# Optimization experiments

Measured on AMD Instinct MI355X. Metric: run time of the kernel, lower is better.

Reference implementation:

```python
import jax, jax.numpy as jnp
import numpy as np

B, S, D = 64, 2048, 512


def setup_inputs() -> dict:
    key = jax.random.key(0)
    ks = jax.random.split(key, 6)
    scale = 1.0 / np.sqrt(D)
    return {
        "source": jax.random.normal(ks[0], (B, D), jnp.float32),
        "memory_bank": jax.random.normal(ks[1], (B, S, D), jnp.float32),
        "memory_lengths": jax.random.randint(ks[2], (B,), 1, S + 1, jnp.int64),
        "Wq": jax.random.normal(ks[3], (D, D), jnp.float32) * scale,
        "bq": jnp.zeros((D,), jnp.float32),
        "Wc": jax.random.normal(ks[4], (D, D), jnp.float32) * scale,
        "v": jax.random.normal(ks[5], (D,), jnp.float32) * scale,
    }


def reference(source, memory_bank, memory_lengths, Wq, bq, Wc, v):
    # Bahdanau (mlp) score: v^T tanh(Wq q + Uc h_j); one_step (tgt_len=1).
    wq = source @ Wq.T + bq                     # [B, D]
    uh = jnp.einsum("bsd,ed->bse", memory_bank, Wc)  # [B, S, D]
    scores = jnp.einsum("bsd,d->bs", jnp.tanh(wq[:, None, :] + uh), v)  # [B, S]
    mask = jnp.arange(S)[None, :] < memory_lengths[:, None]  # [B, S]
    scores = jnp.where(mask, scores, -jnp.inf)
    align = jax.nn.softmax(scores, axis=-1)      # [B, S]
    c = jnp.einsum("bs,bsd->bd", align, memory_bank)  # [B, D] (no_concat=True, mlp -> no tanh)
    return c, align
```

## Files before the change

kernel.cpp:

```cpp
#include <hip/hip_runtime.h>

#define NB 64
#define NS 2048
#define ND 512

typedef short s16x8 __attribute__((ext_vector_type(8)));
typedef float f32x16 __attribute__((ext_vector_type(16)));

__device__ __forceinline__ unsigned short bf16_rnd(float x){
  union { float f; unsigned u; } c; c.f = x;
  unsigned r = c.u + 0x7FFFu + ((c.u >> 16) & 1u);
  return (unsigned short)(r >> 16);
}
__device__ __forceinline__ float bf16f(unsigned short h){
  union { unsigned u; float f; } c; c.u = ((unsigned)h) << 16;
  return c.f;
}
__device__ __forceinline__ float fast_tanh(float x){
  float e = __expf(2.0f * x);
  return 1.0f - 2.0f / (e + 1.0f);
}

__global__ void k_prep_wc(const float* __restrict__ Wc, unsigned short* __restrict__ wcf){
  int t  = blockIdx.x * 256 + threadIdx.x;
  int l  = t & 63;
  int n  = (t >> 6) & 15;
  int ks = t >> 10;
  int e  = n * 32 + (l & 31);
  int d0 = ks * 16 + ((l >> 5) * 8);
  const float4* g4 = (const float4*)(Wc + (size_t)e * ND + d0);
  float4 x0 = g4[0], x1 = g4[1];
  float xs[8] = {x0.x,x0.y,x0.z,x0.w,x1.x,x1.y,x1.z,x1.w};
  s16x8 hv, lv;
#pragma unroll
  for(int j=0;j<8;j++){
    float x = xs[j];
    unsigned short h = bf16_rnd(x);
    hv[j] = (short)h;
    lv[j] = (short)bf16_rnd(x - bf16f(h));
  }
  size_t base = ((size_t)(ks*16 + n))*1024 + (size_t)l*8;
  *(s16x8*)(wcf + base)       = hv;
  *(s16x8*)(wcf + base + 512) = lv;
}

__global__ void k_wq(const float* __restrict__ src, const float* __restrict__ Wq,
                     const float* __restrict__ bq, float* __restrict__ wq){
  __shared__ float s_src[ND];
  int b = blockIdx.x;
  for(int i=threadIdx.x;i<ND;i+=256) s_src[i] = src[(size_t)b*ND + i];
  __syncthreads();
  for(int e=threadIdx.x; e<ND; e+=256){
    const float4* wr = (const float4*)(Wq + (size_t)e*ND);
    float acc = 0.f;
#pragma unroll 4
    for(int i=0;i<ND/4;i++){
      float4 w4 = wr[i];
      acc += w4.x*s_src[4*i] + w4.y*s_src[4*i+1] + w4.z*s_src[4*i+2] + w4.w*s_src[4*i+3];
    }
    wq[(size_t)b*ND + e] = acc + bq[e];
  }
}

__launch_bounds__(512, 2)
__global__ void k_scores(const float* __restrict__ mb, const unsigned short* __restrict__ wcf,
                         const float* __restrict__ wq, const float* __restrict__ v,
                         float* __restrict__ scores){
  __shared__ unsigned short a_lds[2*32*2*64*8];
  __shared__ float wq_s[ND];
  __shared__ float v_s[ND];
  __shared__ float sred[8][64];

  int b  = blockIdx.x >> 5;
  int sc = blockIdx.x & 31;
  int s0 = sc * 64;
  int tid = threadIdx.x;
  int w = tid >> 6;
  int l = tid & 63;

  if(tid < ND){ wq_s[tid] = wq[(size_t)b*ND + tid]; v_s[tid] = v[tid]; }

  const float* mbb = mb + ((size_t)b*NS + s0) * ND;
#pragma unroll
  for(int i=0;i<8;i++){
    int flat = w + 8*i;
    int mt = flat >> 5;
    int ks = flat & 31;
    int r  = mt*32 + (l & 31);
    int k0 = ks*16 + ((l >> 5) * 8);
    const float4* g4 = (const float4*)(mbb + (size_t)r*ND + k0);
    float4 x0 = g4[0], x1 = g4[1];
    float xs[8] = {x0.x,x0.y,x0.z,x0.w,x1.x,x1.y,x1.z,x1.w};
    s16x8 hv, lv;
#pragma unroll
    for(int j=0;j<8;j++){
      float x = xs[j];
      unsigned short h = bf16_rnd(x);
      hv[j] = (short)h;
      lv[j] = (short)bf16_rnd(x - bf16f(h));
    }
    int base = (((mt*32 + ks)*2)*64 + l) * 8;
    *(s16x8*)(a_lds + base)       = hv;
    *(s16x8*)(a_lds + base + 512) = lv;
  }
  __syncthreads();

  const s16x8* aptr = (const s16x8*)a_lds;
  const s16x8* bptr = (const s16x8*)wcf;

  f32x16 acc[2][2];
#pragma unroll
  for(int mt=0;mt<2;mt++)
#pragma unroll
    for(int nt=0;nt<2;nt++)
#pragma unroll
      for(int q=0;q<16;q++) acc[mt][nt][q] = 0.f;

  int n0 = w * 2;
#pragma unroll 2
  for(int ks=0;ks<32;ks++){
    s16x8 a0h = aptr[       ks*128      + l];
    s16x8 a0l = aptr[       ks*128 + 64 + l];
    s16x8 a1h = aptr[4096 + ks*128      + l];
    s16x8 a1l = aptr[4096 + ks*128 + 64 + l];
    const s16x8* bp = bptr + ((size_t)ks*16 + n0)*128 + l;
    s16x8 b0h = bp[0];
    s16x8 b0l = bp[64];
    s16x8 b1h = bp[128];
    s16x8 b1l = bp[192];

    acc[0][0] = __builtin_amdgcn_mfma_f32_32x32x16_bf16(a0h, b0h, acc[0][0], 0,0,0);
    acc[1][0] = __builtin_amdgcn_mfma_f32_32x32x16_bf16(a1h, b0h, acc[1][0], 0,0,0);
    acc[0][1] = __builtin_amdgcn_mfma_f32_32x32x16_bf16(a0h, b1h, acc[0][1], 0,0,0);
    acc[1][1] = __builtin_amdgcn_mfma_f32_32x32x16_bf16(a1h, b1h, acc[1][1], 0,0,0);
    acc[0][0] = __builtin_amdgcn_mfma_f32_32x32x16_bf16(a0h, b0l, acc[0][0], 0,0,0);
    acc[1][0] = __builtin_amdgcn_mfma_f32_32x32x16_bf16(a1h, b0l, acc[1][0], 0,0,0);
    acc[0][1] = __builtin_amdgcn_mfma_f32_32x32x16_bf16(a0h, b1l, acc[0][1], 0,0,0);
    acc[1][1] = __builtin_amdgcn_mfma_f32_32x32x16_bf16(a1h, b1l, acc[1][1], 0,0,0);
    acc[0][0] = __builtin_amdgcn_mfma_f32_32x32x16_bf16(a0l, b0h, acc[0][0], 0,0,0);
    acc[1][0] = __builtin_amdgcn_mfma_f32_32x32x16_bf16(a1l, b0h, acc[1][0], 0,0,0);
    acc[0][1] = __builtin_amdgcn_mfma_f32_32x32x16_bf16(a0l, b1h, acc[0][1], 0,0,0);
    acc[1][1] = __builtin_amdgcn_mfma_f32_32x32x16_bf16(a1l, b1h, acc[1][1], 0,0,0);
  }

  float sp[2][16];
#pragma unroll
  for(int mt=0;mt<2;mt++)
#pragma unroll
    for(int r=0;r<16;r++) sp[mt][r] = 0.f;

#pragma unroll
  for(int nt=0;nt<2;nt++){
    int e = (n0 + nt)*32 + (l & 31);
    float wqe = wq_s[e];
    float ve  = v_s[e];
#pragma unroll
    for(int mt=0;mt<2;mt++)
#pragma unroll
      for(int r=0;r<16;r++){
        float th = fast_tanh(acc[mt][nt][r] + wqe);
        sp[mt][r] += ve * th;
      }
  }

#pragma unroll
  for(int o=1;o<32;o<<=1){
#pragma unroll
    for(int mt=0;mt<2;mt++)
#pragma unroll
      for(int r=0;r<16;r++)
        sp[mt][r] += __shfl_xor(sp[mt][r], o, 64);
  }

  if((l & 31) == 0){
    int half = l >> 5;
#pragma unroll
    for(int mt=0;mt<2;mt++)
#pragma unroll
      for(int r=0;r<16;r++){
        int row = mt*32 + (r&3) + 8*(r>>2) + 4*half;
        sred[w][row] = sp[mt][r];
      }
  }
  __syncthreads();
  if(tid < 64){
    float s = 0.f;
#pragma unroll
    for(int ww=0;ww<8;ww++) s += sred[ww][tid];
    scores[(size_t)b*NS + s0 + tid] = s;
  }
}

__global__ void k_softmax(const float* __restrict__ scores, const unsigned* __restrict__ lraw,
                          float* __restrict__ align){
  __shared__ float red[4];
  int b = blockIdx.x, tid = threadIdx.x;
  bool is64 = (lraw[1] == 0u);
  int len = (int)(is64 ? lraw[2*b] : lraw[b]);

  float loc[8];
  float mx = -1e30f;
#pragma unroll
  for(int i=0;i<8;i++){
    int s = tid + i*256;
    float val = scores[(size_t)b*NS + s];
    loc[i] = (s < len) ? val : -1e30f;
    mx = fmaxf(mx, loc[i]);
  }
#pragma unroll
  for(int o=1;o<64;o<<=1) mx = fmaxf(mx, __shfl_xor(mx, o, 64));
  if((tid & 63) == 0) red[tid >> 6] = mx;
  __syncthreads();
  mx = fmaxf(fmaxf(red[0],red[1]), fmaxf(red[2],red[3]));
  __syncthreads();

  float sum = 0.f;
#pragma unroll
  for(int i=0;i<8;i++){
    int s = tid + i*256;
    loc[i] = (s < len) ? __expf(loc[i] - mx) : 0.f;
    sum += loc[i];
  }
#pragma unroll
  for(int o=1;o<64;o<<=1) sum += __shfl_xor(sum, o, 64);
  if((tid & 63) == 0) red[tid >> 6] = sum;
  __syncthreads();
  sum = red[0] + red[1] + red[2] + red[3];
  float inv = 1.f / sum;
#pragma unroll
  for(int i=0;i<8;i++){
    int s = tid + i*256;
    align[(size_t)b*NS + s] = loc[i] * inv;
  }
}

__global__ void k_context(const float* __restrict__ mb, const float* __restrict__ align,
                          float* __restrict__ c){
  int b  = blockIdx.x >> 4;
  int sc = blockIdx.x & 15;
  int s0 = sc * 128;
  int d0 = threadIdx.x * 2;
  const float* base = mb + ((size_t)b*NS + s0)*ND + d0;
  float a0 = 0.f, a1 = 0.f;
  for(int i=0;i<128;i++){
    float al = align[(size_t)b*NS + s0 + i];
    if(al != 0.f){
      float2 m = *(const float2*)(base + (size_t)i*ND);
      a0 += al * m.x;
      a1 += al * m.y;
    }
  }
  atomicAdd(&c[(size_t)b*ND + d0],     a0);
  atomicAdd(&c[(size_t)b*ND + d0 + 1], a1);
}

extern "C" void kernel_launch(void* const* d_in, const int* in_sizes, int n_in,
                              void* d_out, int out_size, void* d_ws, size_t ws_size,
                              hipStream_t stream) {
  (void)in_sizes; (void)n_in; (void)out_size; (void)ws_size;
  const float*    src  = (const float*)d_in[0];
  const float*    mb   = (const float*)d_in[1];
  const unsigned* lens = (const unsigned*)d_in[2];
  const float*    Wq   = (const float*)d_in[3];
  const float*    bq   = (const float*)d_in[4];
  const float*    Wc   = (const float*)d_in[5];
  const float*    v    = (const float*)d_in[6];

  float* out   = (float*)d_out;
  float* c     = out;
  float* align = out + NB*ND;

  char* ws = (char*)d_ws;
  unsigned short* wcf    = (unsigned short*)ws;
  float*          wq     = (float*)(ws + (1<<20));
  float*          scores = (float*)(ws + (1<<20) + (128<<10));

  hipMemsetAsync(c, 0, NB*ND*sizeof(float), stream);
  k_prep_wc<<<128, 256, 0, stream>>>(Wc, wcf);
  k_wq<<<64, 256, 0, stream>>>(src, Wq, bq, wq);
  k_scores<<<NB*(NS/64), 512, 0, stream>>>(mb, wcf, wq, v, scores);
  k_softmax<<<NB, 256, 0, stream>>>(scores, lens, align);
  k_context<<<NB*16, 256, 0, stream>>>(mb, align, c);
}
```

Baseline: 652.5 us.

## Replace split-bf16 MFMA GEMM with single fp16 MFMA and simplify context kernel

```diff
diff --git a/kernel.cpp b/kernel.cpp
--- a/kernel.cpp
+++ b/kernel.cpp
@@ -4,24 +4,15 @@
 #define NS 2048
 #define ND 512
 
-typedef short s16x8 __attribute__((ext_vector_type(8)));
+typedef _Float16 f16x8 __attribute__((ext_vector_type(8)));
 typedef float f32x16 __attribute__((ext_vector_type(16)));
 
-__device__ __forceinline__ unsigned short bf16_rnd(float x){
-  union { float f; unsigned u; } c; c.f = x;
-  unsigned r = c.u + 0x7FFFu + ((c.u >> 16) & 1u);
-  return (unsigned short)(r >> 16);
-}
-__device__ __forceinline__ float bf16f(unsigned short h){
-  union { unsigned u; float f; } c; c.u = ((unsigned)h) << 16;
-  return c.f;
-}
 __device__ __forceinline__ float fast_tanh(float x){
   float e = __expf(2.0f * x);
   return 1.0f - 2.0f / (e + 1.0f);
 }
 
-__global__ void k_prep_wc(const float* __restrict__ Wc, unsigned short* __restrict__ wcf){
+__global__ void k_prep_wc(const float* __restrict__ Wc, _Float16* __restrict__ wcf){
   int t  = blockIdx.x * 256 + threadIdx.x;
   int l  = t & 63;
   int n  = (t >> 6) & 15;
@@ -31,17 +22,11 @@
   const float4* g4 = (const float4*)(Wc + (size_t)e * ND + d0);
   float4 x0 = g4[0], x1 = g4[1];
   float xs[8] = {x0.x,x0.y,x0.z,x0.w,x1.x,x1.y,x1.z,x1.w};
-  s16x8 hv, lv;
-#pragma unroll
-  for(int j=0;j<8;j++){
-    float x = xs[j];
-    unsigned short h = bf16_rnd(x);
-    hv[j] = (short)h;
-    lv[j] = (short)bf16_rnd(x - bf16f(h));
-  }
-  size_t base = ((size_t)(ks*16 + n))*1024 + (size_t)l*8;
-  *(s16x8*)(wcf + base)       = hv;
-  *(s16x8*)(wcf + base + 512) = lv;
+  f16x8 hv;
+#pragma unroll
+  for(int j=0;j<8;j++) hv[j] = (_Float16)xs[j];
+  size_t base = ((size_t)((ks*16 + n)*64 + l)) * 8;
+  *(f16x8*)(wcf + base) = hv;
 }
 
 __global__ void k_wq(const float* __restrict__ src, const float* __restrict__ Wq,
@@ -62,11 +47,11 @@
   }
 }
 
-__launch_bounds__(512, 2)
-__global__ void k_scores(const float* __restrict__ mb, const unsigned short* __restrict__ wcf,
+__launch_bounds__(512, 4)
+__global__ void k_scores(const float* __restrict__ mb, const _Float16* __restrict__ wcf,
                          const float* __restrict__ wq, const float* __restrict__ v,
                          float* __restrict__ scores){
-  __shared__ unsigned short a_lds[2*32*2*64*8];
+  __shared__ _Float16 a_lds[2*32*64*8];
   __shared__ float wq_s[ND];
   __shared__ float v_s[ND];
   __shared__ float sred[8][64];
@@ -91,22 +76,16 @@
     const float4* g4 = (const float4*)(mbb + (size_t)r*ND + k0);
     float4 x0 = g4[0], x1 = g4[1];
     float xs[8] = {x0.x,x0.y,x0.z,x0.w,x1.x,x1.y,x1.z,x1.w};
-    s16x8 hv, lv;
-#pragma unroll
-    for(int j=0;j<8;j++){
-      float x = xs[j];
-      unsigned short h = bf16_rnd(x);
-      hv[j] = (short)h;
-      lv[j] = (short)bf16_rnd(x - bf16f(h));
-    }
-    int base = (((mt*32 + ks)*2)*64 + l) * 8;
-    *(s16x8*)(a_lds + base)       = hv;
-    *(s16x8*)(a_lds + base + 512) = lv;
-  }
-  __syncthreads();
-
-  const s16x8* aptr = (const s16x8*)a_lds;
-  const s16x8* bptr = (const s16x8*)wcf;
+    f16x8 hv;
+#pragma unroll
+    for(int j=0;j<8;j++) hv[j] = (_Float16)xs[j];
+    int base = ((mt*32 + ks)*64 + l) * 8;
+    *(f16x8*)(a_lds + base) = hv;
+  }
+  __syncthreads();
+
+  const f16x8* aptr = (const f16x8*)a_lds;
+  const f16x8* bptr = (const f16x8*)wcf;
 
   f32x16 acc[2][2];
 #pragma unroll
@@ -117,30 +96,18 @@
       for(int q=0;q<16;q++) acc[mt][nt][q] = 0.f;
 
   int n0 = w * 2;
-#pragma unroll 2
+#pragma unroll 4
   for(int ks=0;ks<32;ks++){
-    s16x8 a0h = aptr[       ks*128      + l];
-    s16x8 a0l = aptr[       ks*128 + 64 + l];
-    s16x8 a1h = aptr[4096 + ks*128      + l];
-    s16x8 a1l = aptr[4096 + ks*128 + 64 + l];
-    const s16x8* bp = bptr + ((size_t)ks*16 + n0)*128 + l;
-    s16x8 b0h = bp[0];
-    s16x8 b0l = bp[64];
-    s16x8 b1h = bp[128];
-    s16x8 b1l = bp[192];
-
-    acc[0][0] = __builtin_amdgcn_mfma_f32_32x32x16_bf16(a0h, b0h, acc[0][0], 0,0,0);
-    acc[1][0] = __builtin_amdgcn_mfma_f32_32x32x16_bf16(a1h, b0h, acc[1][0], 0,0,0);
-    acc[0][1] = __builtin_amdgcn_mfma_f32_32x32x16_bf16(a0h, b1h, acc[0][1], 0,0,0);
-    acc[1][1] = __builtin_amdgcn_mfma_f32_32x32x16_bf16(a1h, b1h, acc[1][1], 0,0,0);
-    acc[0][0] = __builtin_amdgcn_mfma_f32_32x32x16_bf16(a0h, b0l, acc[0][0], 0,0,0);
-    acc[1][0] = __builtin_amdgcn_mfma_f32_32x32x16_bf16(a1h, b0l, acc[1][0], 0,0,0);
-    acc[0][1] = __builtin_amdgcn_mfma_f32_32x32x16_bf16(a0h, b1l, acc[0][1], 0,0,0);
-    acc[1][1] = __builtin_amdgcn_mfma_f32_32x32x16_bf16(a1h, b1l, acc[1][1], 0,0,0);
-    acc[0][0] = __builtin_amdgcn_mfma_f32_32x32x16_bf16(a0l, b0h, acc[0][0], 0,0,0);
-    acc[1][0] = __builtin_amdgcn_mfma_f32_32x32x16_bf16(a1l, b0h, acc[1][0], 0,0,0);
-    acc[0][1] = __builtin_amdgcn_mfma_f32_32x32x16_bf16(a0l, b1h, acc[0][1], 0,0,0);
-    acc[1][1] = __builtin_amdgcn_mfma_f32_32x32x16_bf16(a1l, b1h, acc[1][1], 0,0,0);
+    f16x8 a0 = aptr[       ks*64 + l];
+    f16x8 a1 = aptr[2048 + ks*64 + l];
+    const f16x8* bp = bptr + ((size_t)ks*16 + n0)*64 + l;
+    f16x8 b0 = bp[0];
+    f16x8 b1 = bp[64];
+
+    acc[0][0] = __builtin_amdgcn_mfma_f32_32x32x16_f16(a0, b0, acc[0][0], 0,0,0);
+    acc[1][0] = __builtin_amdgcn_mfma_f32_32x32x16_f16(a1, b0, acc[1][0], 0,0,0);
+    acc[0][1] = __builtin_amdgcn_mfma_f32_32x32x16_f16(a0, b1, acc[0][1], 0,0,0);
+    acc[1][1] = __builtin_amdgcn_mfma_f32_32x32x16_f16(a1, b1, acc[1][1], 0,0,0);
   }
 
   float sp[2][16];
@@ -236,22 +203,20 @@
 
 __global__ void k_context(const float* __restrict__ mb, const float* __restrict__ align,
                           float* __restrict__ c){
+  __shared__ float als[128];
   int b  = blockIdx.x >> 4;
   int sc = blockIdx.x & 15;
   int s0 = sc * 128;
-  int d0 = threadIdx.x * 2;
-  const float* base = mb + ((size_t)b*NS + s0)*ND + d0;
-  float a0 = 0.f, a1 = 0.f;
+  int tid = threadIdx.x;
+  if(tid < 128) als[tid] = align[(size_t)b*NS + s0 + tid];
+  __syncthreads();
+  const float* base = mb + ((size_t)b*NS + s0)*ND + tid;
+  float a = 0.f;
+#pragma unroll 8
   for(int i=0;i<128;i++){
-    float al = align[(size_t)b*NS + s0 + i];
-    if(al != 0.f){
-      float2 m = *(const float2*)(base + (size_t)i*ND);
-      a0 += al * m.x;
-      a1 += al * m.y;
-    }
-  }
-  atomicAdd(&c[(size_t)b*ND + d0],     a0);
-  atomicAdd(&c[(size_t)b*ND + d0 + 1], a1);
+    a += als[i] * base[(size_t)i*ND];
+  }
+  atomicAdd(&c[(size_t)b*ND + tid], a);
 }
 
 extern "C" void kernel_launch(void* const* d_in, const int* in_sizes, int n_in,
@@ -271,14 +236,14 @@
   float* align = out + NB*ND;
 
   char* ws = (char*)d_ws;
-  unsigned short* wcf    = (unsigned short*)ws;
-  float*          wq     = (float*)(ws + (1<<20));
-  float*          scores = (float*)(ws + (1<<20) + (128<<10));
+  _Float16* wcf    = (_Float16*)ws;
+  float*    wq     = (float*)(ws + (512<<10));
+  float*    scores = (float*)(ws + (512<<10) + (128<<10));
 
   hipMemsetAsync(c, 0, NB*ND*sizeof(float), stream);
   k_prep_wc<<<128, 256, 0, stream>>>(Wc, wcf);
   k_wq<<<64, 256, 0, stream>>>(src, Wq, bq, wq);
   k_scores<<<NB*(NS/64), 512, 0, stream>>>(mb, wcf, wq, v, scores);
   k_softmax<<<NB, 256, 0, stream>>>(scores, lens, align);
-  k_context<<<NB*16, 256, 0, stream>>>(mb, align, c);
-}
+  k_context<<<NB*16, 512, 0, stream>>>(mb, align, c);
+}
```

After: 530.0 us. 18.8% less time.
